# Kernel optimization log

Measured on AMD Instinct MI355X. Metric: run time of the kernel, lower is better.

## Reference

```python
import jax, jax.numpy as jnp
import numpy as np

V = 49152      # HEALPix nside=64 pixel count
B = 2
FIN = 32
FOUT = 64
K = 8          # Chebyshev kernel_size
DEG = 8        # neighbors per pixel (plus self-loop -> 9 nnz/row)
G = 8          # GroupNorm num_groups
EPS = 1e-5
SLOPE = 0.1    # LeakyReLU negative slope


def setup_inputs() -> dict:
    key = jax.random.key(0)
    ks = jax.random.split(key, 4)
    rng = np.random.default_rng(0)
    # sparse Laplacian in COO: 8 random neighbors + self-loop per node
    row = np.repeat(np.arange(V, dtype=np.int32), DEG + 1)
    nbrs = rng.integers(0, V, size=(V, DEG))
    col = np.concatenate([nbrs, np.arange(V)[:, None]], axis=1).astype(np.int32).reshape(-1)
    vals = (rng.standard_normal(V * (DEG + 1)).astype(np.float32)) * 0.1
    x = jax.random.normal(ks[0], (B, V, FIN), dtype=jnp.float32)
    W1 = jax.random.normal(ks[1], (K, FIN, FOUT), dtype=jnp.float32) * 0.05
    W2 = jax.random.normal(ks[2], (K, FOUT, FOUT), dtype=jnp.float32) * 0.05
    Wr = jax.random.normal(ks[3], (K, FIN, FOUT), dtype=jnp.float32) * 0.05
    zeros = jnp.zeros((FOUT,), dtype=jnp.float32)
    ones = jnp.ones((FOUT,), dtype=jnp.float32)
    return {
        "x": x,
        "lap_vals": jnp.asarray(vals),
        "lap_row": jnp.asarray(row),
        "lap_col": jnp.asarray(col),
        "W1": W1, "b1": zeros, "g1": ones, "be1": zeros,
        "W2": W2, "b2": zeros, "g2": ones, "be2": zeros,
        "Wr": Wr, "br": zeros,
    }


def _spmm(vals, row, col, z):
    # L @ z for COO Laplacian; z: [V, D]
    return jax.ops.segment_sum(vals[:, None] * z[col], row, num_segments=V)


def _cheb_conv(x, vals, row, col, W, b):
    # x: [B, V, Fin], W: [K, Fin, Fout] -> [B, V, Fout]
    Bb, Vv, F = x.shape
    x0 = jnp.transpose(x, (1, 0, 2)).reshape(Vv, Bb * F)  # [V, B*F]
    xs = [x0, _spmm(vals, row, col, x0)]
    for _ in range(K - 2):
        xs.append(2.0 * _spmm(vals, row, col, xs[-1]) - xs[-2])
    Xk = jnp.stack(xs, 0).reshape(K, Vv, Bb, F)
    Xk = jnp.transpose(Xk, (2, 1, 0, 3))  # [B, V, K, F]
    return jnp.einsum('bvkf,kfo->bvo', Xk, W) + b


def _group_norm(x, gamma, beta):
    # equivalent to nn.GroupNorm applied on x.permute(0,2,1): normalize over (C/G, V)
    Bb, Vv, C = x.shape
    xg = x.reshape(Bb, Vv, G, C // G)
    mu = xg.mean(axis=(1, 3), keepdims=True)
    var = xg.var(axis=(1, 3), keepdims=True)
    xn = ((xg - mu) * jax.lax.rsqrt(var + EPS)).reshape(Bb, Vv, C)
    return xn * gamma + beta


def _block(x, vals, row, col, W, b, gamma, beta):
    h = _cheb_conv(x, vals, row, col, W, b)
    h = _group_norm(h, gamma, beta)
    return jax.nn.leaky_relu(h, SLOPE)  # out_channels > 1 -> LeakyReLU(0.1)


def reference(x, lap_vals, lap_row, lap_col, W1, b1, g1, be1, W2, b2, g2, be2, Wr, br):
    h = _block(x, lap_vals, lap_row, lap_col, W1, b1, g1, be1)
    h = _block(h, lap_vals, lap_row, lap_col, W2, b2, g2, be2)
    res = _cheb_conv(x, lap_vals, lap_row, lap_col, Wr, br)  # in != out -> res_conv
    return h + res
```

## Files before the change

### kernel.cpp

```cpp
#include <hip/hip_runtime.h>
#include <hip/hip_bf16.h>

#define V 49152
#define NNZ 9
#define EPSV 1e-5f
#define SLOPE 0.1f
#define RST 68

typedef __attribute__((ext_vector_type(8))) short bf16x8;
typedef __attribute__((ext_vector_type(4))) float f32x4;

__device__ __forceinline__ float lo2f(unsigned u) { return __uint_as_float(u << 16); }
__device__ __forceinline__ float hi2f(unsigned u) { return __uint_as_float(u & 0xffff0000u); }
__device__ __forceinline__ unsigned short f2us(float f) {
    __hip_bfloat16 h = __float2bfloat16(f);
    return *(unsigned short*)&h;
}
__device__ __forceinline__ unsigned pk2(float a, float b) {
    return ((unsigned)f2us(a)) | (((unsigned)f2us(b)) << 16);
}
__device__ __forceinline__ void fma8(float* t, float a, uint4 u) {
    t[0] += a * lo2f(u.x); t[1] += a * hi2f(u.x);
    t[2] += a * lo2f(u.y); t[3] += a * hi2f(u.y);
    t[4] += a * lo2f(u.z); t[5] += a * hi2f(u.z);
    t[6] += a * lo2f(u.w); t[7] += a * hi2f(u.w);
}
__device__ __forceinline__ void fold8(float* t, uint4 p) {
    t[0] = 2.f*t[0] - lo2f(p.x); t[1] = 2.f*t[1] - hi2f(p.x);
    t[2] = 2.f*t[2] - lo2f(p.y); t[3] = 2.f*t[3] - hi2f(p.y);
    t[4] = 2.f*t[4] - lo2f(p.z); t[5] = 2.f*t[5] - hi2f(p.z);
    t[6] = 2.f*t[6] - lo2f(p.w); t[7] = 2.f*t[7] - hi2f(p.w);
}
__device__ __forceinline__ uint4 pack8(const float* t) {
    uint4 r;
    r.x = pk2(t[0], t[1]); r.y = pk2(t[2], t[3]);
    r.z = pk2(t[4], t[5]); r.w = pk2(t[6], t[7]);
    return r;
}
__device__ __forceinline__ void gnleaky8(uint4 u, const float* scl, const float* sft, float* y) {
    float e[8] = { lo2f(u.x), hi2f(u.x), lo2f(u.y), hi2f(u.y),
                   lo2f(u.z), hi2f(u.z), lo2f(u.w), hi2f(u.w) };
    #pragma unroll
    for (int i = 0; i < 8; ++i) {
        float t = e[i] * scl[i] + sft[i];
        y[i] = t > 0.f ? t : SLOPE * t;
    }
}
__device__ __forceinline__ void gload_lds16(const void* g, void* l) {
    __builtin_amdgcn_global_load_lds((__attribute__((address_space(1))) void*)g,
                                     (__attribute__((address_space(3))) void*)l, 16, 0, 0);
}

#define EPI_PASS(SRCM, PB, BI, DSTPTR, DOSTATS)                                     \
    {                                                                               \
        __syncthreads();                                                            \
        _Pragma("unroll")                                                           \
        for (int m_ = 0; m_ < 4; ++m_)                                              \
            _Pragma("unroll")                                                       \
            for (int rr_ = 0; rr_ < 4; ++rr_) {                                     \
                int r_ = m_ * 16 + quad * 4 + rr_;                                  \
                epi[r_ * RST + o] = SRCM[m_][PB][rr_] + (BI);                       \
            }                                                                       \
        __syncthreads();                                                            \
        _Pragma("unroll")                                                           \
        for (int j_ = 0; j_ < 2; ++j_) {                                            \
            int cid_ = (int)threadIdx.x + 256 * j_;                                 \
            int g_ = cid_ & 7, r_ = cid_ >> 3;                                      \
            const float* src_ = epi + r_ * RST + g_ * 8;                            \
            float e_[8], s_ = 0.f, q_ = 0.f;                                        \
            _Pragma("unroll")                                                       \
            for (int i_ = 0; i_ < 8; ++i_) { e_[i_] = src_[i_]; s_ += e_[i_]; q_ += e_[i_] * e_[i_]; } \
            *(uint4*)(void*)((DSTPTR) + ((size_t)(PB) * V + v0 + r_) * 64 + g_ * 8) = pack8(e_); \
            if (DOSTATS) {                                                          \
                atomicAdd(&sGrp[(PB) * 8 + g_], s_);                                \
                atomicAdd(&sGrp[16 + (PB) * 8 + g_], q_);                           \
            }                                                                       \
        }                                                                           \
    }

__global__ __launch_bounds__(256) void prep_reorder_k(
    const float* __restrict__ x, unsigned* __restrict__ t0,
    const float* __restrict__ W1, const float* __restrict__ Wr, const float* __restrict__ W2,
    unsigned short* __restrict__ Wt1, unsigned short* __restrict__ Wtr, unsigned short* __restrict__ Wt2,
    float* __restrict__ part)
{
    int bid = blockIdx.x;
    if (bid < 6144) {
        int idx = bid * 256 + threadIdx.x;
        int v = idx >> 5, j2 = idx & 31;
        int b = j2 >> 4, f0 = (j2 & 15) * 2;
        const float* p = x + ((size_t)b * V + v) * 32 + f0;
        t0[idx] = pk2(p[0], p[1]);
    } else {
        int i = (bid - 6144) * 256 + threadIdx.x;
        if (i < 32768) {
            int kk = i >> 12, rem = i & 4095, o = rem >> 6, f = rem & 63;
            Wt2[i] = f2us(W2[kk * 4096 + f * 64 + o]);
        } else if (i < 49152) {
            int j = i - 32768;
            int kk = j >> 11, rem = j & 2047, o = rem >> 5, f = rem & 31;
            Wt1[j] = f2us(W1[kk * 2048 + f * 64 + o]);
        } else if (i < 65536) {
            int j = i - 49152;
            int kk = j >> 11, rem = j & 2047, o = rem >> 5, f = rem & 31;
            Wtr[j] = f2us(Wr[kk * 2048 + f * 64 + o]);
        } else if (i < 65600) {
            part[i - 65536] = 0.f;
        }
    }
}

template<int THR, bool FIRST>
__global__ __launch_bounds__(256) void spmm_step(
    const uint4* __restrict__ zc, const uint4* __restrict__ zp, uint4* __restrict__ zn,
    const float* __restrict__ vals, const int* __restrict__ col)
{
    constexpr int L4 = THR * 2;
    int tid = blockIdx.x * 256 + threadIdx.x;
    int v = tid / THR;
    int c = (tid - v * THR) * 2;
    int base = v * NNZ;
    float t[16];
    #pragma unroll
    for (int i = 0; i < 16; ++i) t[i] = 0.f;
    #pragma unroll
    for (int n = 0; n < NNZ; ++n) {
        float a = vals[base + n];
        int cc = col[base + n];
        const uint4* p = zc + (size_t)cc * L4 + c;
        fma8(t, a, p[0]);
        fma8(t + 8, a, p[1]);
    }
    if (!FIRST) {
        const uint4* pp = zp + (size_t)v * L4 + c;
        fold8(t, pp[0]);
        fold8(t + 8, pp[1]);
    }
    uint4* q = zn + (size_t)v * L4 + c;
    q[0] = pack8(t);
    q[1] = pack8(t + 8);
}

#define PPITCH (V * 32)

template<bool ROWOUT>
__global__ __launch_bounds__(256) void spmm2p(
    const unsigned short* __restrict__ zc, const unsigned short* __restrict__ zp,
    unsigned short* __restrict__ zn,
    const float* __restrict__ vals, const int* __restrict__ col)
{
    int p = blockIdx.x & 3;
    int v = (blockIdx.x >> 2) * 64 + (threadIdx.x >> 2);
    int sub = threadIdx.x & 3;
    size_t pb = (size_t)p * PPITCH;
    float t[8];
    #pragma unroll
    for (int i = 0; i < 8; ++i) t[i] = 0.f;
    int base = v * NNZ;
    #pragma unroll
    for (int n = 0; n < NNZ; ++n) {
        float a = vals[base + n];
        int cc = col[base + n];
        uint4 u = *(const uint4*)(const void*)(zc + pb + (size_t)cc * 32 + sub * 8);
        fma8(t, a, u);
    }
    uint4 pz = *(const uint4*)(const void*)(zp + pb + (size_t)v * 32 + sub * 8);
    fold8(t, pz);
    if constexpr (ROWOUT)
        *(uint4*)(void*)(zn + (size_t)v * 128 + p * 32 + sub * 8) = pack8(t);
    else
        *(uint4*)(void*)(zn + pb + (size_t)v * 32 + sub * 8) = pack8(t);
}

template<int MODE>
__global__ __launch_bounds__(256) void spmm2_gn(
    const unsigned short* __restrict__ ACC, const unsigned short* __restrict__ zc,
    unsigned short* __restrict__ zn, const float* __restrict__ part,
    const float* __restrict__ gamma, const float* __restrict__ beta,
    const float* __restrict__ vals, const int* __restrict__ col)
{
    int p = blockIdx.x & 3;
    int v = (blockIdx.x >> 2) * 64 + (threadIdx.x >> 2);
    int sub = threadIdx.x & 3;
    int b = p >> 1;
    int ch0 = (p & 1) * 32 + sub * 8;
    int g = ch0 >> 3, j8 = b * 8 + g;
    const float Nf = (float)V * 8.f;
    float mean = part[j8 * 2] / Nf;
    float rstd = rsqrtf(part[j8 * 2 + 1] / Nf - mean * mean + EPSV);
    float scl[8], sft[8];
    #pragma unroll
    for (int i = 0; i < 8; ++i) {
        scl[i] = rstd * gamma[ch0 + i];
        sft[i] = beta[ch0 + i] - mean * scl[i];
    }
    size_t pb = (size_t)p * PPITCH;

    float t[8];
    #pragma unroll
    for (int i = 0; i < 8; ++i) t[i] = 0.f;
    int base = v * NNZ;
    #pragma unroll
    for (int n = 0; n < NNZ; ++n) {
        float a = vals[base + n];
        int cc = col[base + n];
        if constexpr (MODE == 0) {
            uint4 u = *(const uint4*)(const void*)(ACC + ((size_t)b * V + cc) * 64 + ch0);
            float y[8];
            gnleaky8(u, scl, sft, y);
            #pragma unroll
            for (int i = 0; i < 8; ++i) t[i] += a * y[i];
        } else {
            uint4 u = *(const uint4*)(const void*)(zc + pb + (size_t)cc * 32 + sub * 8);
            fma8(t, a, u);
        }
    }
    if constexpr (MODE == 1) {
        uint4 u = *(const uint4*)(const void*)(ACC + ((size_t)b * V + v) * 64 + ch0);
        float y[8];
        gnleaky8(u, scl, sft, y);
        #pragma unroll
        for (int i = 0; i < 8; ++i) t[i] = 2.f * t[i] - y[i];
    }
    *(uint4*)(void*)(zn + pb + (size_t)v * 32 + sub * 8) = pack8(t);
}

__global__ __launch_bounds__(256) void gemm1f(
    const unsigned short* __restrict__ T,
    const unsigned short* __restrict__ WtA, const unsigned short* __restrict__ WtB,
    const float* __restrict__ biasA, const float* __restrict__ biasB,
    const float* __restrict__ vals, const int* __restrict__ col,
    unsigned short* __restrict__ ACC, unsigned short* __restrict__ RES, float* __restrict__ part)
{
    __shared__ __align__(16) unsigned short shraw[16384];
    __shared__ float sGrp[32];
    float* epi = (float*)shraw;
    unsigned short* bA = shraw;
    unsigned short* bB = shraw + 8192;

    int wv = threadIdx.x >> 6, lane = threadIdx.x & 63;
    int quad = lane >> 4, l15 = lane & 15;
    int v0 = blockIdx.x * 64;
    int ot = wv;

    auto stage = [&](int kk, unsigned short* dst) {
        #pragma unroll
        for (int i = 0; i < 2; ++i) {
            int s = (i * 4 + wv) * 64 + lane;
            int row = s >> 3, cl = s & 7;
            int cg = cl ^ (row & 7);
            const unsigned short* gp = T + ((size_t)kk * V + v0 + row) * 64 + cg * 8;
            gload_lds16(gp, dst + (size_t)(i * 4 + wv) * 64 * 8);
        }
    };

    f32x4 acc[4][2], accd[4][2];
    auto comp = [&](int kk, const unsigned short* sb) {
        size_t brow = ((size_t)kk * 64 + ot * 16 + l15) * 32 + quad * 8;
        bf16x8 w = *(const bf16x8*)(const void*)(WtA + brow);
        bf16x8 d = *(const bf16x8*)(const void*)(WtB + brow);
        #pragma unroll
        for (int m = 0; m < 4; ++m) {
            int r = m * 16 + l15, rx = r & 7;
            const unsigned short* rbase = sb + (size_t)r * 64;
            #pragma unroll
            for (int b = 0; b < 2; ++b) {
                int s0 = (b * 4 + quad) ^ rx;
                bf16x8 a = *(const bf16x8*)(const void*)(rbase + s0 * 8);
                acc[m][b]  = __builtin_amdgcn_mfma_f32_16x16x32_bf16(a, w, acc[m][b], 0, 0, 0);
                accd[m][b] = __builtin_amdgcn_mfma_f32_16x16x32_bf16(a, d, accd[m][b], 0, 0, 0);
            }
        }
    };

    stage(0, bA); stage(1, bA + 4096);
    #pragma unroll
    for (int m = 0; m < 4; ++m)
        #pragma unroll
        for (int b = 0; b < 2; ++b) {
            acc[m][b]  = (f32x4){0.f, 0.f, 0.f, 0.f};
            accd[m][b] = (f32x4){0.f, 0.f, 0.f, 0.f};
        }
    __syncthreads();

    stage(2, bB); stage(3, bB + 4096);
    comp(0, bA); comp(1, bA + 4096);
    __syncthreads();

    stage(4, bA); stage(5, bA + 4096);
    comp(2, bB); comp(3, bB + 4096);
    __syncthreads();

    stage(6, bB);
    {
        const unsigned short* T6 = T + (size_t)6 * V * 64;
        const unsigned short* T5 = T + (size_t)5 * V * 64;
        int row = threadIdx.x >> 2, c2 = (threadIdx.x & 3) * 2;
        int gv = v0 + row;
        float t[16];
        #pragma unroll
        for (int i = 0; i < 16; ++i) t[i] = 0.f;
        int base = gv * NNZ;
        #pragma unroll
        for (int n = 0; n < NNZ; ++n) {
            float a = vals[base + n];
            int cc = col[base + n];
            const uint4* p = (const uint4*)(const void*)(T6 + (size_t)cc * 64 + c2 * 8);
            fma8(t, a, p[0]);
            fma8(t + 8, a, p[1]);
        }
        const uint4* pp = (const uint4*)(const void*)(T5 + (size_t)gv * 64 + c2 * 8);
        fold8(t, pp[0]);
        fold8(t + 8, pp[1]);
        uint4* tl = (uint4*)(bB + 4096);
        int r7 = row & 7;
        comp(4, bA); comp(5, bA + 4096);
        tl[row * 8 + (c2 ^ r7)]       = pack8(t);
        tl[row * 8 + ((c2 + 1) ^ r7)] = pack8(t + 8);
    }
    __syncthreads();

    comp(6, bB); comp(7, bB + 4096);

    if (threadIdx.x < 32) sGrp[threadIdx.x] = 0.f;
    int o = ot * 16 + l15;
    float biA = biasA[o], biB = biasB[o];
    EPI_PASS(acc,  0, biA, ACC, true)
    EPI_PASS(acc,  1, biA, ACC, true)
    EPI_PASS(accd, 0, biB, RES, false)
    EPI_PASS(accd, 1, biB, RES, false)
    __syncthreads();
    if (threadIdx.x < 16) {
        atomicAdd(&part[threadIdx.x * 2],     sGrp[threadIdx.x]);
        atomicAdd(&part[threadIdx.x * 2 + 1], sGrp[16 + threadIdx.x]);
    }
}

__global__ __launch_bounds__(256) void gemm2f(
    const unsigned short* __restrict__ T,
    unsigned short* ACC,
    const float* __restrict__ part1, const float* __restrict__ g1, const float* __restrict__ be1,
    const unsigned short* __restrict__ Wt2, const float* __restrict__ biasA,
    float* __restrict__ part2,
    const float* __restrict__ vals, const int* __restrict__ col)
{
    __shared__ __align__(16) unsigned short shraw[16384];
    __shared__ float sGrp[32];
    float* epi = (float*)shraw;
    unsigned short* b0 = shraw;
    unsigned short* b1 = shraw + 8192;

    int wv = threadIdx.x >> 6, lane = threadIdx.x & 63;
    int quad = lane >> 4, l15 = lane & 15;
    int v0 = blockIdx.x * 64;
    int ot = wv;
    const float Nf = (float)V * 8.f;

    auto stage = [&](int kk, unsigned short* dst, bool rowm) {
        #pragma unroll
        for (int i = 0; i < 4; ++i) {
            int s = (i * 4 + wv) * 64 + lane;
            int row = (s >> 2) & 63, panel = s >> 8, slot = s & 3;
            int sub = slot ^ (row & 3);
            const unsigned short* gp = rowm
                ? T + (size_t)kk * (V * 128) + (size_t)(v0 + row) * 128 + panel * 32 + sub * 8
                : T + (size_t)kk * (V * 128) + (size_t)panel * PPITCH
                    + (size_t)(v0 + row) * 32 + sub * 8;
            gload_lds16(gp, dst + (size_t)(i * 4 + wv) * 64 * 8);
        }
    };

    f32x4 acc[4][2];
    auto comp = [&](int kk, const unsigned short* sb) {
        size_t brow = ((size_t)kk * 64 + ot * 16 + l15) * 64 + quad * 8;
        bf16x8 w0 = *(const bf16x8*)(const void*)(Wt2 + brow);
        bf16x8 w1 = *(const bf16x8*)(const void*)(Wt2 + brow + 32);
        #pragma unroll
        for (int m = 0; m < 4; ++m) {
            int r = m * 16 + l15;
            #pragma unroll
            for (int b = 0; b < 2; ++b)
                #pragma unroll
                for (int fh = 0; fh < 2; ++fh) {
                    int pos = (b * 2 + fh) * 256 + r * 4 + (quad ^ (r & 3));
                    bf16x8 a = *(const bf16x8*)(const void*)(sb + (size_t)pos * 8);
                    acc[m][b] = __builtin_amdgcn_mfma_f32_16x16x32_bf16(
                        a, fh ? w1 : w0, acc[m][b], 0, 0, 0);
                }
        }
    };

    stage(1, b1, false);
    {
        int c = threadIdx.x & 15;
        int b = c >> 3, g = c & 7, j8 = b * 8 + g;
        float mean = part1[j8 * 2] / Nf;
        float rstd = rsqrtf(part1[j8 * 2 + 1] / Nf - mean * mean + EPSV);
        int o0 = g * 8;
        float scl[8], sft[8];
        #pragma unroll
        for (int i = 0; i < 8; ++i) {
            scl[i] = rstd * g1[o0 + i];
            sft[i] = be1[o0 + i] - mean * scl[i];
        }
        #pragma unroll
        for (int j = 0; j < 4; ++j) {
            int r = (threadIdx.x >> 4) + 16 * j;
            uint4 aa = *(const uint4*)(const void*)(ACC + ((size_t)b * V + v0 + r) * 64 + o0);
            float y[8];
            gnleaky8(aa, scl, sft, y);
            int pos = (c >> 2) * 256 + r * 4 + ((c & 3) ^ (r & 3));
            *(uint4*)(void*)(b0 + (size_t)pos * 8) = pack8(y);
        }
    }
    #pragma unroll
    for (int m = 0; m < 4; ++m)
        #pragma unroll
        for (int b = 0; b < 2; ++b) acc[m][b] = (f32x4){0.f, 0.f, 0.f, 0.f};
    __syncthreads();

    comp(0, b0);
    __syncthreads();
    stage(2, b0, false); comp(1, b1);
    __syncthreads();
    stage(3, b1, false); comp(2, b0);
    __syncthreads();
    stage(4, b0, false); comp(3, b1);
    __syncthreads();
    stage(5, b1, false); comp(4, b0);
    __syncthreads();
    stage(6, b0, true);  comp(5, b1);
    __syncthreads();
    {
        const unsigned short* T6 = T + (size_t)6 * V * 128;
        const unsigned short* T5 = T + (size_t)5 * V * 128;
        int row = threadIdx.x >> 2, p = threadIdx.x & 3;
        int gv = v0 + row;
        size_t pb = (size_t)p * PPITCH;
        float t[8 * 4];
        #pragma unroll
        for (int i = 0; i < 32; ++i) t[i] = 0.f;
        int base = gv * NNZ;
        #pragma unroll
        for (int n = 0; n < NNZ; ++n) {
            float a = vals[base + n];
            int cc = col[base + n];
            const uint4* q = (const uint4*)(const void*)(T6 + (size_t)cc * 128 + p * 32);
            fma8(t, a, q[0]);
            fma8(t + 8, a, q[1]);
            fma8(t + 16, a, q[2]);
            fma8(t + 24, a, q[3]);
        }
        const uint4* pz = (const uint4*)(const void*)(T5 + pb + (size_t)gv * 32);
        fold8(t, pz[0]);
        fold8(t + 8, pz[1]);
        fold8(t + 16, pz[2]);
        fold8(t + 24, pz[3]);
        comp(6, b0);
        #pragma unroll
        for (int sub = 0; sub < 4; ++sub) {
            int pos = p * 256 + row * 4 + (sub ^ (row & 3));
            *(uint4*)(void*)(b1 + (size_t)pos * 8) = pack8(t + sub * 8);
        }
    }
    __syncthreads();
    comp(7, b1);

    if (threadIdx.x < 32) sGrp[threadIdx.x] = 0.f;
    int o = ot * 16 + l15;
    float biA = biasA[o];
    EPI_PASS(acc, 0, biA, ACC, true)
    EPI_PASS(acc, 1, biA, ACC, true)
    __syncthreads();
    if (threadIdx.x < 16) {
        atomicAdd(&part2[threadIdx.x * 2],     sGrp[threadIdx.x]);
        atomicAdd(&part2[threadIdx.x * 2 + 1], sGrp[16 + threadIdx.x]);
    }
}

__global__ __launch_bounds__(256) void final_out(const unsigned short* __restrict__ ACC,
                                                 const unsigned short* __restrict__ RES,
                                                 float* __restrict__ out,
                                                 const float* __restrict__ part,
                                                 const float* __restrict__ gamma, const float* __restrict__ beta) {
    int idx = blockIdx.x * 256 + threadIdx.x;
    int b = idx >= V * 8 ? 1 : 0;
    int r = idx - b * V * 8;
    int v = r >> 3, g = r & 7;
    int j = b * 8 + g;
    const float N = (float)V * 8.f;
    float mean = part[j * 2] / N;
    float rstd = rsqrtf(part[j * 2 + 1] / N - mean * mean + EPSV);
    int o0 = g * 8;
    size_t base = ((size_t)b * V + v) * 64 + o0;
    uint4 aa = *(const uint4*)(const void*)(ACC + base);
    uint4 rr = *(const uint4*)(const void*)(RES + base);
    float e[8] = { lo2f(aa.x), hi2f(aa.x), lo2f(aa.y), hi2f(aa.y),
                   lo2f(aa.z), hi2f(aa.z), lo2f(aa.w), hi2f(aa.w) };
    float re[8] = { lo2f(rr.x), hi2f(rr.x), lo2f(rr.y), hi2f(rr.y),
                    lo2f(rr.z), hi2f(rr.z), lo2f(rr.w), hi2f(rr.w) };
    float y[8];
    #pragma unroll
    for (int i = 0; i < 8; ++i) {
        float t = (e[i] - mean) * rstd * gamma[o0 + i] + beta[o0 + i];
        y[i] = (t > 0.f ? t : SLOPE * t) + re[i];
    }
    float4 w0 = { y[0], y[1], y[2], y[3] };
    float4 w1 = { y[4], y[5], y[6], y[7] };
    *(float4*)(void*)(out + base) = w0;
    *(float4*)(void*)(out + base + 4) = w1;
}

extern "C" void kernel_launch(void* const* d_in, const int* in_sizes, int n_in,
                              void* d_out, int out_size, void* d_ws, size_t ws_size,
                              hipStream_t stream) {
    const float* x    = (const float*)d_in[0];
    const float* vals = (const float*)d_in[1];
    const int*   col  = (const int*)d_in[3];
    const float* W1   = (const float*)d_in[4];
    const float* b1   = (const float*)d_in[5];
    const float* g1   = (const float*)d_in[6];
    const float* be1  = (const float*)d_in[7];
    const float* W2   = (const float*)d_in[8];
    const float* b2   = (const float*)d_in[9];
    const float* g2   = (const float*)d_in[10];
    const float* be2  = (const float*)d_in[11];
    const float* Wr   = (const float*)d_in[12];
    const float* br   = (const float*)d_in[13];
    float* out = (float*)d_out;

    unsigned short* TS  = (unsigned short*)d_ws;
    unsigned short* ACC = TS + (size_t)8 * V * 128;
    unsigned short* RES = ACC + (size_t)2 * V * 64;
    unsigned short* Wt1 = RES + (size_t)2 * V * 64;
    unsigned short* Wtr = Wt1 + 8 * 64 * 32;
    unsigned short* Wt2 = Wtr + 8 * 64 * 32;
    float* PART1 = (float*)(Wt2 + 8 * 64 * 64);
    float* PART2 = PART1 + 32;

    prep_reorder_k<<<6404, 256, 0, stream>>>(x, (unsigned*)TS, W1, Wr, W2, Wt1, Wtr, Wt2, PART1);

    uint4* T1s[8];
    for (int k = 0; k < 8; ++k) T1s[k] = (uint4*)(TS + (size_t)k * V * 64);
    spmm_step<4, true><<<V * 4 / 256, 256, 0, stream>>>(T1s[0], nullptr, T1s[1], vals, col);
    for (int k = 2; k < 7; ++k)
        spmm_step<4, false><<<V * 4 / 256, 256, 0, stream>>>(T1s[k-1], T1s[k-2], T1s[k], vals, col);

    gemm1f<<<V / 64, 256, 0, stream>>>(TS, Wt1, Wtr, b1, br, vals, col, ACC, RES, PART1);

    unsigned short* T2s[8];
    for (int k = 0; k < 8; ++k) T2s[k] = TS + (size_t)k * V * 128;
    spmm2_gn<0><<<4 * V / 64, 256, 0, stream>>>(ACC, nullptr, T2s[1], PART1, g1, be1, vals, col);
    spmm2_gn<1><<<4 * V / 64, 256, 0, stream>>>(ACC, T2s[1], T2s[2], PART1, g1, be1, vals, col);
    for (int k = 3; k < 6; ++k)
        spmm2p<false><<<4 * V / 64, 256, 0, stream>>>(T2s[k-1], T2s[k-2], T2s[k], vals, col);
    spmm2p<true><<<4 * V / 64, 256, 0, stream>>>(T2s[5], T2s[4], T2s[6], vals, col);

    gemm2f<<<V / 64, 256, 0, stream>>>(TS, ACC, PART1, g1, be1, Wt2, b2, PART2, vals, col);

    final_out<<<2 * V * 8 / 256, 256, 0, stream>>>(ACC, RES, out, PART2, g2, be2);
}
```

Measured before the change: 352.4 us.

## Split layer-1 Chebyshev SpMM into two column panels for gather locality

The first-block Chebyshev recurrence now stores intermediate T_k in two 32-column panel-major buffers instead of 64-column rows. Each SpMM launch handles one panel per block, so the random neighbor gathers touch a smaller working set and may hit cache more often. T0 and T6 stay row-major, and the GEMM staging, swizzle and fold addressing are rewritten to read the mixed layouts. This adds layout bookkeeping and more, smaller thread work items, each loading 16 bytes per neighbor instead of 32.

```diff
diff --git a/kernel.cpp b/kernel.cpp
--- a/kernel.cpp
+++ b/kernel.cpp
@@ -110,35 +110,41 @@
     }
 }
 
-template<int THR, bool FIRST>
-__global__ __launch_bounds__(256) void spmm_step(
-    const uint4* __restrict__ zc, const uint4* __restrict__ zp, uint4* __restrict__ zn,
+#define PP1 (V * 32)
+
+template<int SRCROW, int FOLDROW, int ROWOUT, int FIRST>
+__global__ __launch_bounds__(256) void spmm1p(
+    const unsigned short* __restrict__ zc, const unsigned short* __restrict__ zp,
+    unsigned short* __restrict__ zn,
     const float* __restrict__ vals, const int* __restrict__ col)
 {
-    constexpr int L4 = THR * 2;
-    int tid = blockIdx.x * 256 + threadIdx.x;
-    int v = tid / THR;
-    int c = (tid - v * THR) * 2;
+    int p = blockIdx.x & 1;
+    int v = (blockIdx.x >> 1) * 64 + (threadIdx.x >> 2);
+    int sub = threadIdx.x & 3;
+    size_t pb = (size_t)p * PP1;
+    float t[8];
+    #pragma unroll
+    for (int i = 0; i < 8; ++i) t[i] = 0.f;
     int base = v * NNZ;
-    float t[16];
-    #pragma unroll
-    for (int i = 0; i < 16; ++i) t[i] = 0.f;
     #pragma unroll
     for (int n = 0; n < NNZ; ++n) {
         float a = vals[base + n];
         int cc = col[base + n];
-        const uint4* p = zc + (size_t)cc * L4 + c;
-        fma8(t, a, p[0]);
-        fma8(t + 8, a, p[1]);
-    }
-    if (!FIRST) {
-        const uint4* pp = zp + (size_t)v * L4 + c;
-        fold8(t, pp[0]);
-        fold8(t + 8, pp[1]);
-    }
-    uint4* q = zn + (size_t)v * L4 + c;
-    q[0] = pack8(t);
-    q[1] = pack8(t + 8);
+        const unsigned short* src = SRCROW
+            ? zc + (size_t)cc * 64 + p * 32 + sub * 8
+            : zc + pb + (size_t)cc * 32 + sub * 8;
+        fma8(t, a, *(const uint4*)(const void*)src);
+    }
+    if constexpr (!FIRST) {
+        const unsigned short* fp = FOLDROW
+            ? zp + (size_t)v * 64 + p * 32 + sub * 8
+            : zp + pb + (size_t)v * 32 + sub * 8;
+        fold8(t, *(const uint4*)(const void*)fp);
+    }
+    unsigned short* dst = ROWOUT
+        ? zn + (size_t)v * 64 + p * 32 + sub * 8
+        : zn + pb + (size_t)v * 32 + sub * 8;
+    *(uint4*)(void*)dst = pack8(t);
 }
 
 #define PPITCH (V * 32)
@@ -243,13 +249,16 @@
     int v0 = blockIdx.x * 64;
     int ot = wv;
 
-    auto stage = [&](int kk, unsigned short* dst) {
+    auto stage = [&](int kk, unsigned short* dst, bool rowm) {
         #pragma unroll
         for (int i = 0; i < 2; ++i) {
             int s = (i * 4 + wv) * 64 + lane;
-            int row = s >> 3, cl = s & 7;
-            int cg = cl ^ (row & 7);
-            const unsigned short* gp = T + ((size_t)kk * V + v0 + row) * 64 + cg * 8;
+            int row = (s >> 2) & 63, panel = s >> 8, slot = s & 3;
+            int sub = slot ^ (row & 3);
+            const unsigned short* gp = rowm
+                ? T + (size_t)kk * (V * 64) + (size_t)(v0 + row) * 64 + panel * 32 + sub * 8
+                : T + (size_t)kk * (V * 64) + (size_t)panel * PP1
+                    + (size_t)(v0 + row) * 32 + sub * 8;
             gload_lds16(gp, dst + (size_t)(i * 4 + wv) * 64 * 8);
         }
     };
@@ -261,19 +270,18 @@
         bf16x8 d = *(const bf16x8*)(const void*)(WtB + brow);
         #pragma unroll
         for (int m = 0; m < 4; ++m) {
-            int r = m * 16 + l15, rx = r & 7;
-            const unsigned short* rbase = sb + (size_t)r * 64;
+            int r = m * 16 + l15;
             #pragma unroll
             for (int b = 0; b < 2; ++b) {
-                int s0 = (b * 4 + quad) ^ rx;
-                bf16x8 a = *(const bf16x8*)(const void*)(rbase + s0 * 8);
+                int pos = b * 256 + r * 4 + (quad ^ (r & 3));
+                bf16x8 a = *(const bf16x8*)(const void*)(sb + (size_t)pos * 8);
                 acc[m][b]  = __builtin_amdgcn_mfma_f32_16x16x32_bf16(a, w, acc[m][b], 0, 0, 0);
                 accd[m][b] = __builtin_amdgcn_mfma_f32_16x16x32_bf16(a, d, accd[m][b], 0, 0, 0);
             }
         }
     };
 
-    stage(0, bA); stage(1, bA + 4096);
+    stage(0, bA, true); stage(1, bA + 4096, false);
     #pragma unroll
     for (int m = 0; m < 4; ++m)
         #pragma unroll
@@ -283,15 +291,15 @@
         }
     __syncthreads();
 
-    stage(2, bB); stage(3, bB + 4096);
+    stage(2, bB, false); stage(3, bB + 4096, false);
     comp(0, bA); comp(1, bA + 4096);
     __syncthreads();
 
-    stage(4, bA); stage(5, bA + 4096);
+    stage(4, bA, false); stage(5, bA + 4096, false);
     comp(2, bB); comp(3, bB + 4096);
     __syncthreads();
 
-    stage(6, bB);
+    stage(6, bB, true);
     {
         const unsigned short* T6 = T + (size_t)6 * V * 64;
         const unsigned short* T5 = T + (size_t)5 * V * 64;
@@ -309,14 +317,18 @@
             fma8(t, a, p[0]);
             fma8(t + 8, a, p[1]);
         }
-        const uint4* pp = (const uint4*)(const void*)(T5 + (size_t)gv * 64 + c2 * 8);
+        const uint4* pp = (const uint4*)(const void*)
+            (T5 + (size_t)(c2 >> 2) * PP1 + (size_t)gv * 32 + (c2 & 3) * 8);
         fold8(t, pp[0]);
         fold8(t + 8, pp[1]);
         uint4* tl = (uint4*)(bB + 4096);
-        int r7 = row & 7;
         comp(4, bA); comp(5, bA + 4096);
-        tl[row * 8 + (c2 ^ r7)]       = pack8(t);
-        tl[row * 8 + ((c2 + 1) ^ r7)] = pack8(t + 8);
+        #pragma unroll
+        for (int q = 0; q < 2; ++q) {
+            int c = c2 + q;
+            int pos = (c >> 2) * 256 + row * 4 + ((c & 3) ^ (row & 3));
+            tl[pos] = pack8(t + q * 8);
+        }
     }
     __syncthreads();
 
@@ -540,11 +552,13 @@
 
     prep_reorder_k<<<6404, 256, 0, stream>>>(x, (unsigned*)TS, W1, Wr, W2, Wt1, Wtr, Wt2, PART1);
 
-    uint4* T1s[8];
-    for (int k = 0; k < 8; ++k) T1s[k] = (uint4*)(TS + (size_t)k * V * 64);
-    spmm_step<4, true><<<V * 4 / 256, 256, 0, stream>>>(T1s[0], nullptr, T1s[1], vals, col);
-    for (int k = 2; k < 7; ++k)
-        spmm_step<4, false><<<V * 4 / 256, 256, 0, stream>>>(T1s[k-1], T1s[k-2], T1s[k], vals, col);
+    unsigned short* T1s[8];
+    for (int k = 0; k < 8; ++k) T1s[k] = TS + (size_t)k * V * 64;
+    spmm1p<1,0,0,1><<<2 * V / 64, 256, 0, stream>>>(T1s[0], nullptr, T1s[1], vals, col);
+    spmm1p<0,1,0,0><<<2 * V / 64, 256, 0, stream>>>(T1s[1], T1s[0], T1s[2], vals, col);
+    for (int k = 3; k < 6; ++k)
+        spmm1p<0,0,0,0><<<2 * V / 64, 256, 0, stream>>>(T1s[k-1], T1s[k-2], T1s[k], vals, col);
+    spmm1p<0,0,1,0><<<2 * V / 64, 256, 0, stream>>>(T1s[5], T1s[4], T1s[6], vals, col);
 
     gemm1f<<<V / 64, 256, 0, stream>>>(TS, Wt1, Wtr, b1, br, vals, col, ACC, RES, PART1);
 
```

Measured after the change: 358.3 us. Within noise of the previous version (+1.7%).
